# Optimization experiments

Measured on AMD Instinct MI355X. Metric: run time of the kernel, lower is better.

## Reference

```python
import jax, jax.numpy as jnp
import numpy as np

GRID = (160, 160, 160)
RADIUS_FACTOR = 3.0
PATCH = 20      # fixed patch edge; covers ceil(c+r)-floor(c-r)+1 for r <= 9 voxels
CHUNK = 500
N_POINTS = 25000


def _quat_to_rot(q):
    # normalized quaternion -> rotation matrix (matches torch reference)
    q = q / jnp.clip(jnp.linalg.norm(q, axis=-1, keepdims=True), 1e-6)
    w, x, y, z = q[..., 0], q[..., 1], q[..., 2], q[..., 3]
    ww, xx, yy, zz = w * w, x * x, y * y, z * z
    wx, wy, wz = w * x, w * y, w * z
    xy, xz, yz = x * y, x * z, y * z
    r0 = jnp.stack([ww + xx - yy - zz, 2 * (xy - wz), 2 * (xz + wy)], -1)
    r1 = jnp.stack([2 * (xy + wz), ww - xx + yy - zz, 2 * (yz - wx)], -1)
    r2 = jnp.stack([2 * (xz - wy), 2 * (yz + wx), ww - xx - yy + zz], -1)
    return jnp.stack([r0, r1, r2], -2)


def setup_inputs():
    key = jax.random.key(0)
    k1, k2, k3, k4 = jax.random.split(key, 4)
    centers = jax.random.uniform(k1, (N_POINTS, 3), dtype=jnp.float32)
    # scales in [1.5, 3.0] voxels -> patch radius = 3*max(scale) <= 9 < PATCH/2
    log_scales = jnp.log(jax.random.uniform(k2, (N_POINTS, 3), minval=1.5, maxval=3.0, dtype=jnp.float32))
    quats = jax.random.normal(k3, (N_POINTS, 4), dtype=jnp.float32)
    rho = 0.1 * jax.random.normal(k4, (N_POINTS, 2), dtype=jnp.float32)  # (real, imag)
    return {"centers": centers, "log_scales": log_scales, "quats": quats, "rho": rho}


def _splat(centers, log_scales, quats, rho):
    D, H, W = GRID
    span = jnp.array([D - 1, H - 1, W - 1], jnp.float32)
    scales = jnp.exp(log_scales)                                  # [N,3]
    R = _quat_to_rot(quats)                                       # [N,3,3]
    inv = 1.0 / jnp.clip(scales, 1e-4) ** 2                       # diag of S^-2
    prec = jnp.einsum('nij,nj,nkj->nik', R, inv, R)               # R diag R^T, [N,3,3]
    cv = centers * span                                           # voxel-space centers
    rad = jnp.max(scales, axis=-1) * RADIUS_FACTOR                # per-point patch radius
    base = jnp.floor(cv - rad[:, None]).astype(jnp.int32)         # zmin/ymin/xmin (pre-clip)
    hi = jnp.ceil(cv + rad[:, None]).astype(jnp.int32)            # zmax/ymax/xmax (pre-clip)
    amp_mag = jnp.sqrt(rho[:, 0] ** 2 + rho[:, 1] ** 2)
    valid = (amp_mag >= 1e-6) & (rad >= 1e-3)                     # torch skip conditions
    dims = jnp.array([D, H, W], jnp.int32)

    nchunk = N_POINTS // CHUNK
    ck = lambda a: a.reshape((nchunk, CHUNK) + a.shape[1:])
    xs = (ck(cv), ck(base), ck(hi), ck(prec), ck(rho), ck(valid))
    offs = jnp.arange(PATCH, dtype=jnp.int32)

    def step(vol, x):
        cv_c, base_c, hi_c, p, rho_c, val_c = x
        idx = base_c[:, :, None] + offs                           # [C,3,P] voxel indices
        d = idx.astype(jnp.float32) - cv_c[:, :, None]            # [C,3,P] rel coords
        m = (idx >= 0) & (idx < dims[None, :, None]) & (idx <= hi_c[:, :, None])
        dz, dy, dx = d[:, 0], d[:, 1], d[:, 2]                    # [C,P] each
        # exponent = rel^T prec rel, built separably (prec is symmetric)
        e = ((p[:, 0, 0, None] * dz * dz)[:, :, None, None]
             + (p[:, 1, 1, None] * dy * dy)[:, None, :, None]
             + (p[:, 2, 2, None] * dx * dx)[:, None, None, :]
             + (2.0 * p[:, 0, 1, None, None] * dz[:, :, None] * dy[:, None, :])[:, :, :, None]
             + (2.0 * p[:, 0, 2, None, None] * dz[:, :, None] * dx[:, None, :])[:, :, None, :]
             + (2.0 * p[:, 1, 2, None, None] * dy[:, :, None] * dx[:, None, :])[:, None, :, :])
        w = jnp.exp(-0.5 * e)                                     # [C,P,P,P]
        mask = (m[:, 0, :, None, None] & m[:, 1, None, :, None] & m[:, 2, None, None, :]
                & val_c[:, None, None, None])
        w = jnp.where(mask, w, 0.0)
        iz = jnp.clip(idx[:, 0], 0, D - 1)
        iy = jnp.clip(idx[:, 1], 0, H - 1)
        ix = jnp.clip(idx[:, 2], 0, W - 1)
        lin = (iz[:, :, None, None] * H + iy[:, None, :, None]) * W + ix[:, None, None, :]
        contrib = w[..., None] * rho_c[:, None, None, None, :]    # [C,P,P,P,2] (re,im)
        vol = vol.at[lin.reshape(-1)].add(contrib.reshape(-1, 2))
        return vol, None

    vol, _ = jax.lax.scan(step, jnp.zeros((D * H * W, 2), jnp.float32), xs)
    return vol.reshape(D, H, W, 2)


def reference(centers, log_scales, quats, rho):
    return _splat(centers, log_scales, quats, rho)
```

## Files before the change

### kernel.cpp

```cpp
#include <hip/hip_runtime.h>


namespace {
constexpr int GD = 160, GH = 160, GW = 160;
constexpr int NPTS = 25000;
constexpr int PATCH = 20;
constexpr int TS  = 8;
constexpr int TPD = GD / TS;
constexpr int NT  = TPD * TPD * TPD;
constexpr int CAP = 384;
constexpr int PSTRIDE = 16;
constexpr float L2E = 1.4426950408889634f;
}


__global__ void prep_params(const float* __restrict__ centers,
                            const float* __restrict__ log_scales,
                            const float* __restrict__ quats,
                            const float* __restrict__ rho,
                            float* __restrict__ params)
{
    const int gid = blockIdx.x * blockDim.x + threadIdx.x;
    if (gid >= NPTS) return;

    const float r0 = rho[gid * 2 + 0];
    const float r1 = rho[gid * 2 + 1];
    const float s0 = __expf(log_scales[gid * 3 + 0]);
    const float s1 = __expf(log_scales[gid * 3 + 1]);
    const float s2 = __expf(log_scales[gid * 3 + 2]);

    const float smax = fmaxf(s0, fmaxf(s1, s2));
    const float rad  = smax * 3.0f;
    const float amp2 = r0 * r0 + r1 * r1;

    const float cvz = centers[gid * 3 + 0] * (float)(GD - 1);
    const float cvy = centers[gid * 3 + 1] * (float)(GH - 1);
    const float cvx = centers[gid * 3 + 2] * (float)(GW - 1);

    const int bz = (int)floorf(cvz - rad);
    const int by = (int)floorf(cvy - rad);
    const int bx = (int)floorf(cvx - rad);
    const int hz = (int)ceilf(cvz + rad);
    const int hy = (int)ceilf(cvy + rad);
    const int hx = (int)ceilf(cvx + rad);

    const int loz = max(bz, 0), upz = min(min(hz, GD - 1), bz + PATCH - 1);
    const int loy = max(by, 0), upy = min(min(hy, GH - 1), by + PATCH - 1);
    const int lox = max(bx, 0), upx = min(min(hx, GW - 1), bx + PATCH - 1);

    const bool valid = (amp2 >= 1e-12f) && (rad >= 1e-3f) &&
                       (upz >= loz) && (upy >= loy) && (upx >= lox);

    const float q0 = quats[gid * 4 + 0], q1 = quats[gid * 4 + 1];
    const float q2 = quats[gid * 4 + 2], q3 = quats[gid * 4 + 3];
    float qn = sqrtf(q0 * q0 + q1 * q1 + q2 * q2 + q3 * q3);
    qn = fmaxf(qn, 1e-6f);
    const float w = q0 / qn, x = q1 / qn, y = q2 / qn, z = q3 / qn;

    const float R00 = w * w + x * x - y * y - z * z;
    const float R01 = 2.f * (x * y - w * z);
    const float R02 = 2.f * (x * z + w * y);
    const float R10 = 2.f * (x * y + w * z);
    const float R11 = w * w - x * x + y * y - z * z;
    const float R12 = 2.f * (y * z - w * x);
    const float R20 = 2.f * (x * z - w * y);
    const float R21 = 2.f * (y * z + w * x);
    const float R22 = w * w - x * x - y * y + z * z;

    const float c0 = fmaxf(s0, 1e-4f); const float i0 = 1.f / (c0 * c0);
    const float c1 = fmaxf(s1, 1e-4f); const float i1 = 1.f / (c1 * c1);
    const float c2 = fmaxf(s2, 1e-4f); const float i2 = 1.f / (c2 * c2);

    const float p00 = R00 * R00 * i0 + R01 * R01 * i1 + R02 * R02 * i2;
    const float p01 = R00 * R10 * i0 + R01 * R11 * i1 + R02 * R12 * i2;
    const float p02 = R00 * R20 * i0 + R01 * R21 * i1 + R02 * R22 * i2;
    const float p11 = R10 * R10 * i0 + R11 * R11 * i1 + R12 * R12 * i2;
    const float p12 = R10 * R20 * i0 + R11 * R21 * i1 + R12 * R22 * i2;
    const float p22 = R20 * R20 * i0 + R21 * R21 * i1 + R22 * R22 * i2;

    const float q00s = -0.5f * L2E * p00;
    const float v    = __builtin_amdgcn_exp2f(2.f * q00s);

    const int zl = valid ? loz : 255, zu = valid ? upz : 0;
    const int yl = valid ? loy : 255, yu = valid ? upy : 0;
    const int xl = valid ? lox : 255, xu = valid ? upx : 0;
    const int loPack = zl | (yl << 8) | (xl << 16) | (zu << 24);
    const int upPack = yu | (xu << 8);

    float4* P = reinterpret_cast<float4*>(params + (size_t)gid * PSTRIDE);
    P[0] = make_float4(q00s, -L2E * p01, -L2E * p02, -0.5f * L2E * p11);
    P[1] = make_float4(-L2E * p12, -0.5f * L2E * p22, cvz, cvy);
    P[2] = make_float4(cvx, r0, r1, __int_as_float(loPack));
    P[3] = make_float4(__int_as_float(upPack), v, 0.f, 0.f);
}

__global__ __launch_bounds__(256) void bin(const float* __restrict__ params,
                                           int* __restrict__ counts,
                                           unsigned short* __restrict__ list)
{
    const int t = blockIdx.x * 256 + threadIdx.x;
    const int gid  = t >> 6;
    const int lane = t & 63;
    const int lo = __float_as_int(params[(size_t)gid * PSTRIDE + 11]);
    const int up = __float_as_int(params[(size_t)gid * PSTRIDE + 12]);
    const int tz0 = (lo & 255) >> 3,         tz1 = ((lo >> 24) & 255) >> 3;
    const int ty0 = ((lo >> 8) & 255) >> 3,  ty1 = (up & 255) >> 3;
    const int tx0 = ((lo >> 16) & 255) >> 3, tx1 = ((up >> 8) & 255) >> 3;
    const int tz = tz0 + (lane >> 4);
    const int ty = ty0 + ((lane >> 2) & 3);
    const int tx = tx0 + (lane & 3);
    if (tz > tz1 || ty > ty1 || tx > tx1) return;
    const int tile = (tz * TPD + ty) * TPD + tx;
    const int pos = atomicAdd(&counts[tile], 1);
    if (pos < CAP) list[(size_t)tile * CAP + pos] = (unsigned short)gid;
}

__global__ __launch_bounds__(64) void gather(
    const float* __restrict__ params,
    const int* __restrict__ counts,
    const unsigned short* __restrict__ list,
    float2* __restrict__ out)
{
    const int tile = blockIdx.x;
    const int tz = tile / (TPD * TPD);
    const int rem = tile - tz * (TPD * TPD);
    const int ty = rem / TPD;
    const int tx = rem - ty * TPD;

    const int lane = threadIdx.x;
    const int ly = lane >> 3, lx = lane & 7;
    const int iy = ty * TS + ly;
    const int ix = tx * TS + lx;
    const int z0 = tz * TS;
    const float fy = (float)iy, fx = (float)ix, fz = (float)z0;

    __shared__ float4 sP[64][4];

    int cnt = counts[tile];
    if (cnt > CAP) cnt = CAP;
    const float4* p4 = reinterpret_cast<const float4*>(params);
    const unsigned short* tl = list + (size_t)tile * CAP;

    float ar[8], ai[8];
#pragma unroll
    for (int i = 0; i < 8; ++i) { ar[i] = 0.f; ai[i] = 0.f; }

    for (int b0 = 0; b0 < cnt; b0 += 64) {
        const int nb = min(64, cnt - b0);
        __syncthreads();
        if (lane < nb) {
            const int gid = tl[b0 + lane];
            const float4* src = p4 + (size_t)gid * 4;
            sP[lane][0] = src[0];
            sP[lane][1] = src[1];
            sP[lane][2] = src[2];
            sP[lane][3] = src[3];
        }
        __syncthreads();

        for (int g = 0; g < nb; ++g) {
            const float4 Pa = sP[g][0];
            const float4 Pb = sP[g][1];
            const float4 Pc = sP[g][2];
            const float4 Pd = sP[g][3];
            const int lo = __float_as_int(Pc.w);
            const int up = __float_as_int(Pd.x);
            const int loy_ = (lo >> 8) & 255, lox_ = (lo >> 16) & 255;
            const int upy_ = up & 255,        upx_ = (up >> 8) & 255;
            if (iy < loy_ || iy > upy_ || ix < lox_ || ix > upx_) continue;
            const int zl = (lo & 255) - z0;
            const int zu = ((lo >> 24) & 255) - z0;

            const float dy = fy - Pb.w;
            const float dx = fx - Pc.x;
            const float C = fmaf(dy, fmaf(Pa.w, dy, Pb.x * dx), Pb.y * dx * dx);
            const float B = fmaf(Pa.y, dy, Pa.z * dx);
            const float dz = fz - Pb.z;
            const float t0 = fmaf(dz, fmaf(Pa.x, dz, B), C);
            const float dt = fmaf(Pa.x, fmaf(2.f, dz, 1.f), B);
            float w = __builtin_amdgcn_exp2f(t0);
            float u = __builtin_amdgcn_exp2f(dt);
            const float v = Pd.y;
            const float r0 = Pc.y, r1 = Pc.z;
#pragma unroll
            for (int i = 0; i < 8; ++i) {
                const float wm = (i >= zl && i <= zu) ? w : 0.f;
                ar[i] = fmaf(wm, r0, ar[i]);
                ai[i] = fmaf(wm, r1, ai[i]);
                w *= u;
                u *= v;
            }
        }
    }

#pragma unroll
    for (int i = 0; i < 8; ++i)
        out[((size_t)(z0 + i) * GH + iy) * GW + ix] = make_float2(ar[i], ai[i]);
}

extern "C" void kernel_launch(void* const* d_in, const int* in_sizes, int n_in,
                              void* d_out, int out_size, void* d_ws, size_t ws_size,
                              hipStream_t stream) {
    const float* centers    = (const float*)d_in[0];
    const float* log_scales = (const float*)d_in[1];
    const float* quats      = (const float*)d_in[2];
    const float* rho        = (const float*)d_in[3];

    float* params = (float*)d_ws;
    int* counts = (int*)(params + (size_t)NPTS * PSTRIDE);
    unsigned short* list = (unsigned short*)(counts + NT);

    hipMemsetAsync(counts, 0, NT * sizeof(int), stream);
    prep_params<<<(NPTS + 255) / 256, 256, 0, stream>>>(centers, log_scales,
                                                        quats, rho, params);
    bin<<<(NPTS * 64) / 256, 256, 0, stream>>>(params, counts, list);
    gather<<<NT, 64, 0, stream>>>(params, counts, list, (float2*)d_out);
}
```

Measured before the change: 175.7 us.

## Fuse param prep into binning and drop shared staging in gather

Merges prep_params and bin into one kernel where each of 64 lanes per point recomputes the point parameters redundantly, lane 0 writes them, and all lanes bin directly without reading params back. The gather kernel now packs four tiles per 256-thread block, one wave per tile, and reads each point's parameters straight from global memory using a wave-uniform index instead of staging them through shared memory with barriers. This removes a kernel launch, a global round trip and the syncthreads, at the cost of 64x redundant prep math and scalar-load latency per point in the gather loop.

```diff
diff --git a/kernel.cpp b/kernel.cpp
--- a/kernel.cpp
+++ b/kernel.cpp
@@ -14,14 +14,18 @@
 }
 
 
-__global__ void prep_params(const float* __restrict__ centers,
-                            const float* __restrict__ log_scales,
-                            const float* __restrict__ quats,
-                            const float* __restrict__ rho,
-                            float* __restrict__ params)
+__global__ __launch_bounds__(256) void prep_bin(
+    const float* __restrict__ centers,
+    const float* __restrict__ log_scales,
+    const float* __restrict__ quats,
+    const float* __restrict__ rho,
+    float* __restrict__ params,
+    int* __restrict__ counts,
+    unsigned short* __restrict__ list)
 {
-    const int gid = blockIdx.x * blockDim.x + threadIdx.x;
-    if (gid >= NPTS) return;
+    const int t = blockIdx.x * 256 + threadIdx.x;
+    const int gid  = t >> 6;
+    const int lane = t & 63;
 
     const float r0 = rho[gid * 2 + 0];
     const float r1 = rho[gid * 2 + 1];
@@ -87,25 +91,19 @@
     const int loPack = zl | (yl << 8) | (xl << 16) | (zu << 24);
     const int upPack = yu | (xu << 8);
 
-    float4* P = reinterpret_cast<float4*>(params + (size_t)gid * PSTRIDE);
-    P[0] = make_float4(q00s, -L2E * p01, -L2E * p02, -0.5f * L2E * p11);
-    P[1] = make_float4(-L2E * p12, -0.5f * L2E * p22, cvz, cvy);
-    P[2] = make_float4(cvx, r0, r1, __int_as_float(loPack));
-    P[3] = make_float4(__int_as_float(upPack), v, 0.f, 0.f);
-}
-
-__global__ __launch_bounds__(256) void bin(const float* __restrict__ params,
-                                           int* __restrict__ counts,
-                                           unsigned short* __restrict__ list)
-{
-    const int t = blockIdx.x * 256 + threadIdx.x;
-    const int gid  = t >> 6;
-    const int lane = t & 63;
-    const int lo = __float_as_int(params[(size_t)gid * PSTRIDE + 11]);
-    const int up = __float_as_int(params[(size_t)gid * PSTRIDE + 12]);
-    const int tz0 = (lo & 255) >> 3,         tz1 = ((lo >> 24) & 255) >> 3;
-    const int ty0 = ((lo >> 8) & 255) >> 3,  ty1 = (up & 255) >> 3;
-    const int tx0 = ((lo >> 16) & 255) >> 3, tx1 = ((up >> 8) & 255) >> 3;
+    if (lane == 0) {
+        float4* P = reinterpret_cast<float4*>(params + (size_t)gid * PSTRIDE);
+        P[0] = make_float4(q00s, -L2E * p01, -L2E * p02, -0.5f * L2E * p11);
+        P[1] = make_float4(-L2E * p12, -0.5f * L2E * p22, cvz, cvy);
+        P[2] = make_float4(cvx, r0, r1, __int_as_float(loPack));
+        P[3] = make_float4(__int_as_float(upPack), v, 0.f, 0.f);
+    }
+
+    if (!valid) return;
+
+    const int tz0 = loz >> 3, tz1 = upz >> 3;
+    const int ty0 = loy >> 3, ty1 = upy >> 3;
+    const int tx0 = lox >> 3, tx1 = upx >> 3;
     const int tz = tz0 + (lane >> 4);
     const int ty = ty0 + ((lane >> 2) & 3);
     const int tx = tx0 + (lane & 3);
@@ -115,27 +113,26 @@
     if (pos < CAP) list[(size_t)tile * CAP + pos] = (unsigned short)gid;
 }
 
-__global__ __launch_bounds__(64) void gather(
+__global__ __launch_bounds__(256) void gather(
     const float* __restrict__ params,
     const int* __restrict__ counts,
     const unsigned short* __restrict__ list,
     float2* __restrict__ out)
 {
-    const int tile = blockIdx.x;
+    const int wli  = threadIdx.x >> 6;
+    const int tile = __builtin_amdgcn_readfirstlane(blockIdx.x * 4 + wli);
     const int tz = tile / (TPD * TPD);
     const int rem = tile - tz * (TPD * TPD);
     const int ty = rem / TPD;
     const int tx = rem - ty * TPD;
 
-    const int lane = threadIdx.x;
+    const int lane = threadIdx.x & 63;
     const int ly = lane >> 3, lx = lane & 7;
     const int iy = ty * TS + ly;
     const int ix = tx * TS + lx;
     const int z0 = tz * TS;
     const float fy = (float)iy, fx = (float)ix, fz = (float)z0;
 
-    __shared__ float4 sP[64][4];
-
     int cnt = counts[tile];
     if (cnt > CAP) cnt = CAP;
     const float4* p4 = reinterpret_cast<const float4*>(params);
@@ -145,51 +142,38 @@
 #pragma unroll
     for (int i = 0; i < 8; ++i) { ar[i] = 0.f; ai[i] = 0.f; }
 
-    for (int b0 = 0; b0 < cnt; b0 += 64) {
-        const int nb = min(64, cnt - b0);
-        __syncthreads();
-        if (lane < nb) {
-            const int gid = tl[b0 + lane];
-            const float4* src = p4 + (size_t)gid * 4;
-            sP[lane][0] = src[0];
-            sP[lane][1] = src[1];
-            sP[lane][2] = src[2];
-            sP[lane][3] = src[3];
-        }
-        __syncthreads();
-
-        for (int g = 0; g < nb; ++g) {
-            const float4 Pa = sP[g][0];
-            const float4 Pb = sP[g][1];
-            const float4 Pc = sP[g][2];
-            const float4 Pd = sP[g][3];
-            const int lo = __float_as_int(Pc.w);
-            const int up = __float_as_int(Pd.x);
-            const int loy_ = (lo >> 8) & 255, lox_ = (lo >> 16) & 255;
-            const int upy_ = up & 255,        upx_ = (up >> 8) & 255;
-            if (iy < loy_ || iy > upy_ || ix < lox_ || ix > upx_) continue;
-            const int zl = (lo & 255) - z0;
-            const int zu = ((lo >> 24) & 255) - z0;
-
-            const float dy = fy - Pb.w;
-            const float dx = fx - Pc.x;
-            const float C = fmaf(dy, fmaf(Pa.w, dy, Pb.x * dx), Pb.y * dx * dx);
-            const float B = fmaf(Pa.y, dy, Pa.z * dx);
-            const float dz = fz - Pb.z;
-            const float t0 = fmaf(dz, fmaf(Pa.x, dz, B), C);
-            const float dt = fmaf(Pa.x, fmaf(2.f, dz, 1.f), B);
-            float w = __builtin_amdgcn_exp2f(t0);
-            float u = __builtin_amdgcn_exp2f(dt);
-            const float v = Pd.y;
-            const float r0 = Pc.y, r1 = Pc.z;
+    for (int g = 0; g < cnt; ++g) {
+        const int gid = __builtin_amdgcn_readfirstlane((int)tl[g]);
+        const float4 Pa = p4[(size_t)gid * 4 + 0];
+        const float4 Pb = p4[(size_t)gid * 4 + 1];
+        const float4 Pc = p4[(size_t)gid * 4 + 2];
+        const float4 Pd = p4[(size_t)gid * 4 + 3];
+        const int lo = __float_as_int(Pc.w);
+        const int up = __float_as_int(Pd.x);
+        const int loy_ = (lo >> 8) & 255, lox_ = (lo >> 16) & 255;
+        const int upy_ = up & 255,        upx_ = (up >> 8) & 255;
+        if (iy < loy_ || iy > upy_ || ix < lox_ || ix > upx_) continue;
+        const int zl = (lo & 255) - z0;
+        const int zu = ((lo >> 24) & 255) - z0;
+
+        const float dy = fy - Pb.w;
+        const float dx = fx - Pc.x;
+        const float C = fmaf(dy, fmaf(Pa.w, dy, Pb.x * dx), Pb.y * dx * dx);
+        const float B = fmaf(Pa.y, dy, Pa.z * dx);
+        const float dz = fz - Pb.z;
+        const float t0 = fmaf(dz, fmaf(Pa.x, dz, B), C);
+        const float dt = fmaf(Pa.x, fmaf(2.f, dz, 1.f), B);
+        float wgt = __builtin_amdgcn_exp2f(t0);
+        float u   = __builtin_amdgcn_exp2f(dt);
+        const float v = Pd.y;
+        const float r0 = Pc.y, r1 = Pc.z;
 #pragma unroll
-            for (int i = 0; i < 8; ++i) {
-                const float wm = (i >= zl && i <= zu) ? w : 0.f;
-                ar[i] = fmaf(wm, r0, ar[i]);
-                ai[i] = fmaf(wm, r1, ai[i]);
-                w *= u;
-                u *= v;
-            }
+        for (int i = 0; i < 8; ++i) {
+            const float wm = (i >= zl && i <= zu) ? wgt : 0.f;
+            ar[i] = fmaf(wm, r0, ar[i]);
+            ai[i] = fmaf(wm, r1, ai[i]);
+            wgt *= u;
+            u *= v;
         }
     }
 
@@ -211,8 +195,7 @@
     unsigned short* list = (unsigned short*)(counts + NT);
 
     hipMemsetAsync(counts, 0, NT * sizeof(int), stream);
-    prep_params<<<(NPTS + 255) / 256, 256, 0, stream>>>(centers, log_scales,
-                                                        quats, rho, params);
-    bin<<<(NPTS * 64) / 256, 256, 0, stream>>>(params, counts, list);
-    gather<<<NT, 64, 0, stream>>>(params, counts, list, (float2*)d_out);
-}
+    prep_bin<<<(NPTS * 64) / 256, 256, 0, stream>>>(centers, log_scales, quats,
+                                                    rho, params, counts, list);
+    gather<<<NT / 4, 256, 0, stream>>>(params, counts, list, (float2*)d_out);
+}
```

New measurement: 191.8 us. 1.09x slower.
